# Optimization experiments

Hardware: AMD Instinct MI355X
Metric: run time of the kernel (lower is better)

The kernel has to match this reference:

```python
import jax, jax.numpy as jnp
import numpy as np

F = 39          # total fields = 13 numeric + 26 categorical
NUM_NUM = 13
N_CAT = 26
V = 100000      # vocab per categorical field
E = 16          # embed size
RED = max(1, F // 3)  # SE reduction size = 13
P = F * (F - 1) // 2  # 741 pairs
HID = [1024, 512, 256]
B = 4096

I_IDX, J_IDX = np.triu_indices(F, k=1)  # static pair indices, len P


def setup_inputs() -> dict:
    key = jax.random.key(0)
    ks = jax.random.split(key, 16)
    s = 0.01
    inp = {
        "cat": jax.random.randint(ks[0], (B, N_CAT), 0, V),
        "num": jax.random.normal(ks[1], (B, NUM_NUM), dtype=jnp.float32),
        "embed_tables": jax.random.normal(ks[2], (N_CAT, V, E), dtype=jnp.float32) * s,
        "num_emb": jax.random.normal(ks[3], (NUM_NUM, E), dtype=jnp.float32) * s,
        "W_se1": jax.random.normal(ks[4], (F, RED), dtype=jnp.float32) * 0.1,
        "W_se2": jax.random.normal(ks[5], (RED, F), dtype=jnp.float32) * 0.1,
        "W_bil": jax.random.normal(ks[6], (F, E, E), dtype=jnp.float32) * 0.1,  # per-field Linear(E,E,no bias), [field,in,out]
        "W_d1": jax.random.normal(ks[7], (2 * P * E, HID[0]), dtype=jnp.float32) * 0.01,
        "b_d1": jnp.zeros((HID[0],), dtype=jnp.float32),
        "W_d2": jax.random.normal(ks[8], (HID[0], HID[1]), dtype=jnp.float32) * 0.02,
        "b_d2": jnp.zeros((HID[1],), dtype=jnp.float32),
        "W_d3": jax.random.normal(ks[9], (HID[1], HID[2]), dtype=jnp.float32) * 0.02,
        "b_d3": jnp.zeros((HID[2],), dtype=jnp.float32),
        "W_out": jax.random.normal(ks[10], (HID[2], 1), dtype=jnp.float32) * 0.02,
        "b_out": jnp.zeros((1,), dtype=jnp.float32),
    }
    return inp


def _bilinear_each(x, W_bil):
    # x: [B,F,E]; project each field with its own matrix, then pairwise multiply.
    proj = jnp.einsum("bfe,fed->bfd", x, W_bil)            # [B,F,E]
    return proj[:, I_IDX, :] * x[:, J_IDX, :]               # [B,P,E]


def reference(cat, num, embed_tables, num_emb, W_se1, W_se2, W_bil,
              W_d1, b_d1, W_d2, b_d2, W_d3, b_d3, W_out, b_out):
    # categorical embeddings: per-field gather -> [B, N_CAT, E]
    cat_embed = embed_tables[jnp.arange(N_CAT)[None, :], cat]
    # numerical "embeddings": value * learned vector -> [B, NUM_NUM, E]
    num_embed = num[:, :, None] * num_emb[None, :, :]
    x = jnp.concatenate([num_embed, cat_embed], axis=1)     # [B,F,E]

    # SENET gating
    Z = jnp.mean(x, axis=-1)                                 # [B,F]
    A = jax.nn.relu(jax.nn.relu(Z @ W_se1) @ W_se2)          # [B,F]
    V = x * A[:, :, None]

    se_bi = _bilinear_each(V, W_bil)                         # [B,P,E]
    bi = _bilinear_each(x, W_bil)                            # [B,P,E]
    hid = jnp.concatenate([se_bi, bi], axis=1).reshape(x.shape[0], -1)  # [B, 2*P*E]

    h = jax.nn.relu(hid @ W_d1 + b_d1)
    h = jax.nn.relu(h @ W_d2 + b_d2)
    h = jax.nn.relu(h @ W_d3 + b_d3)
    return h @ W_out + b_out                                 # [B,1]
```

## Files before the change

### kernel.cpp

```cpp
#include <hip/hip_runtime.h>

typedef unsigned short u16;
typedef __attribute__((ext_vector_type(8))) __bf16 bf16x8;
typedef __attribute__((ext_vector_type(4))) float f32x4;
typedef __attribute__((ext_vector_type(4))) unsigned short u16x4;
typedef __attribute__((ext_vector_type(8))) unsigned short u16x8;

#define NF    39
#define NNUM  13
#define NCAT  26
#define VOC   100000
#define NPAIR 741
#define KHID  23712
#define BATCH 4096
#define HD1   1024
#define HD2   512
#define HD3   256

__device__ __forceinline__ u16 f2bf(float f) {
  unsigned u = __builtin_bit_cast(unsigned, f);
  return (u16)((u + 0x7fffu + ((u >> 16) & 1u)) >> 16);
}

__device__ __forceinline__ void gload16(const void* g, void* l) {
  __builtin_amdgcn_global_load_lds((const __attribute__((address_space(1))) void*)g,
                                   (__attribute__((address_space(3))) void*)l, 16, 0, 0);
}

__global__ __launch_bounds__(256) void fuse_front(
    const int* __restrict__ cat, const float* __restrict__ num,
    const float* __restrict__ tables, const float* __restrict__ nemb,
    const float* __restrict__ Wse1, const float* __restrict__ Wse2,
    const float* __restrict__ Wbil, u16* __restrict__ hid)
{
  __shared__ float xs[2][NF][16];
  __shared__ float wb[NF][16][16];
  __shared__ float pr[2][NF][16];
  __shared__ float Zs[2][NF], Ts[2][NNUM], As[2][NF];
  __shared__ unsigned char pis[NPAIR], pjs[NPAIR];

  const int b0 = blockIdx.x * 2;
  const int tid = threadIdx.x;

  for (int i = tid; i < NF * 64; i += 256)
    ((f32x4*)wb)[i] = ((const f32x4*)Wbil)[i];

  for (int t = tid; t < 2 * NNUM * 16; t += 256) {
    int r = t / (NNUM * 16), t2 = t % (NNUM * 16);
    int f = t2 >> 4, e = t2 & 15;
    xs[r][f][e] = num[(b0 + r) * NNUM + f] * nemb[t2];
  }
  for (int t = tid; t < 2 * NCAT * 16; t += 256) {
    int r = t / (NCAT * 16), t2 = t % (NCAT * 16);
    int c = t2 >> 4, e = t2 & 15;
    int cv = cat[(b0 + r) * NCAT + c];
    xs[r][NNUM + c][e] = tables[((size_t)c * VOC + cv) * 16 + e];
  }
  for (int p = tid; p < NPAIR; p += 256) {
    int i = 0, rs = 0;
    while (p >= rs + (NF - 1 - i)) { rs += NF - 1 - i; ++i; }
    pis[p] = (unsigned char)i;
    pjs[p] = (unsigned char)(i + 1 + (p - rs));
  }
  __syncthreads();

  if (tid < 2 * NF) {
    int r = tid / NF, f = tid % NF;
    float s = 0.f;
    #pragma unroll
    for (int e = 0; e < 16; ++e) s += xs[r][f][e];
    Zs[r][f] = s * (1.f / 16.f);
  }
  __syncthreads();
  if (tid < 2 * NNUM) {
    int r = tid / NNUM, o = tid % NNUM;
    float s = 0.f;
    for (int f = 0; f < NF; ++f) s += Zs[r][f] * Wse1[f * NNUM + o];
    Ts[r][o] = fmaxf(s, 0.f);
  }
  __syncthreads();
  if (tid < 2 * NF) {
    int r = tid / NF, f = tid % NF;
    float s = 0.f;
    for (int q = 0; q < NNUM; ++q) s += Ts[r][q] * Wse2[q * NF + f];
    As[r][f] = fmaxf(s, 0.f);
  }
  for (int t = tid; t < 2 * NF * 16; t += 256) {
    int r = t / (NF * 16), t2 = t % (NF * 16);
    int f = t2 >> 4, d = t2 & 15;
    float s = 0.f;
    #pragma unroll
    for (int e = 0; e < 16; ++e) s += xs[r][f][e] * wb[f][e][d];
    pr[r][f][d] = s;
  }
  __syncthreads();

  for (int idx = tid; idx < 2 * NPAIR * 2; idx += 256) {
    const int r = idx / (NPAIR * 2), idx2 = idx % (NPAIR * 2);
    const int p = idx2 >> 1, e0 = (idx2 & 1) * 8;
    const int i = pis[p], j = pjs[p];
    const float aa = As[r][i] * As[r][j];
    u16* hr = hid + (size_t)(b0 + r) * KHID;
    u16x8 vb, vs;
    #pragma unroll
    for (int e = 0; e < 8; ++e) {
      float bv = pr[r][i][e0 + e] * xs[r][j][e0 + e];
      vb[e] = f2bf(bv);
      vs[e] = f2bf(aa * bv);
    }
    *reinterpret_cast<u16x8*>(hr + NPAIR * 16 + p * 16 + e0) = vb;
    *reinterpret_cast<u16x8*>(hr + p * 16 + e0) = vs;
  }
}

__global__ __launch_bounds__(256) void transpose_all(
    const float* __restrict__ Wd1, const float* __restrict__ Wd2,
    const float* __restrict__ Wd3, u16* __restrict__ W1t,
    u16* __restrict__ W2t, u16* __restrict__ W3t)
{
  __shared__ float t[32][33];
  const int bid = blockIdx.x;
  const float* in; u16* out; int K, N, kb, nb;
  if (bid < 741 * 32)        { in = Wd1; out = W1t; K = KHID; N = HD1; kb = bid % 741; nb = bid / 741; }
  else if (bid < 741 * 32 + 512) { int r = bid - 741 * 32; in = Wd2; out = W2t; K = HD1; N = HD2; kb = r % 32; nb = r / 32; }
  else                       { int r = bid - 741 * 32 - 512; in = Wd3; out = W3t; K = HD2; N = HD3; kb = r % 16; nb = r / 16; }

  const int k0 = kb * 32, n0 = nb * 32;
  const int c = threadIdx.x & 31, r = threadIdx.x >> 5;
  #pragma unroll
  for (int it = 0; it < 4; ++it)
    t[r + it * 8][c] = in[(size_t)(k0 + r + it * 8) * N + n0 + c];
  __syncthreads();
  const int n = threadIdx.x >> 3, kq = (threadIdx.x & 7) * 4;
  u16x4 v;
  #pragma unroll
  for (int q = 0; q < 4; ++q) v[q] = f2bf(t[kq + q][n]);
  *reinterpret_cast<u16x4*>(out + (size_t)(n0 + n) * K + k0 + kq) = v;
}

__global__ __launch_bounds__(512, 2) void gemm8p_bf16(
    const u16* __restrict__ A, const u16* __restrict__ Bt,
    float* __restrict__ Cp, int M, int N, int K, int totku, int kpb)
{
  __shared__ __align__(16) u16 lds[65536];

  const int tid = threadIdx.x;
  const int wid = tid >> 6, lane = tid & 63;

  const int d = blockIdx.x;
  const int x = d & 7, jj = d >> 3;
  const int mb = ((x & 3) << 2) | (jj & 3);
  const int nb = (jj >> 2) & 3;
  const int sb = ((x >> 2) << 1) | (jj >> 4);

  const int ks0 = sb * kpb;
  const int kunits = (totku - ks0 < kpb) ? (totku - ks0) : kpb;
  const int ftiles = kunits >> 1;

  const int wm = wid >> 2, wn = wid & 3;
  const int lrow = lane & 15, c0 = lane >> 4;

  const int rr = tid >> 2, cc = tid & 3, csrc = cc ^ ((rr >> 1) & 3);
  const u16* pAg = A  + (size_t)((size_t)mb * 256 + rr) * K + (size_t)ks0 * 32 + csrc * 8;
  const u16* pBg = Bt + (size_t)((size_t)nb * 256 + rr) * K + (size_t)ks0 * 32 + csrc * 8;
  const size_t rsk = (size_t)128 * K;
  const int dstoff = tid * 8;

  int offA[8], offB[4];
  #pragma unroll
  for (int m = 0; m < 8; ++m) {
    int r = wm * 128 + m * 16 + lrow;
    offA[m] = r * 32 + ((c0 ^ ((r >> 1) & 3)) << 3);
  }
  #pragma unroll
  for (int n = 0; n < 4; ++n) {
    int r = wn * 64 + n * 16 + lrow;
    offB[n] = r * 32 + ((c0 ^ ((r >> 1) & 3)) << 3);
  }

#define STAGE_A(g) { int sg = ((g) < kunits) ? (g) : (kunits - 1);          \
    const u16* s_ = pAg + (size_t)sg * 32;                                   \
    u16* dp_ = lds + (((g) & 3) * 8192) + dstoff;                            \
    gload16(s_, dp_); gload16(s_ + rsk, dp_ + 4096); }
#define STAGE_B(g) { int sg = ((g) < kunits) ? (g) : (kunits - 1);          \
    const u16* s_ = pBg + (size_t)sg * 32;                                   \
    u16* dp_ = lds + 32768 + (((g) & 3) * 8192) + dstoff;                    \
    gload16(s_, dp_); gload16(s_ + rsk, dp_ + 4096); }

  f32x4 acc[8][4];
  #pragma unroll
  for (int m = 0; m < 8; ++m)
    #pragma unroll
    for (int n = 0; n < 4; ++n) acc[m][n] = f32x4{0.f, 0.f, 0.f, 0.f};

  STAGE_A(0); STAGE_B(0); STAGE_A(1); STAGE_B(1); STAGE_A(2); STAGE_B(2); STAGE_B(3);
  asm volatile("s_waitcnt vmcnt(6)" ::: "memory");
  __builtin_amdgcn_s_barrier();

  bf16x8 a0, a1, a2, a3, bg0, bg1, bg2, bg3;

  for (int tt = 0; tt < ftiles; ++tt) {
    const int g0 = tt << 1;
    const u16* As0 = lds + ((g0 & 3) * 8192);
    const u16* As1 = lds + (((g0 + 1) & 3) * 8192);
    const u16* Bs0 = lds + 32768 + ((g0 & 3) * 8192);
    const u16* Bs1 = lds + 32768 + (((g0 + 1) & 3) * 8192);

    a0 = *reinterpret_cast<const bf16x8*>(As0 + offA[0]);
    a1 = *reinterpret_cast<const bf16x8*>(As0 + offA[1]);
    a2 = *reinterpret_cast<const bf16x8*>(As0 + offA[2]);
    a3 = *reinterpret_cast<const bf16x8*>(As0 + offA[3]);
    bg0 = *reinterpret_cast<const bf16x8*>(Bs0 + offB[0]);
    bg1 = *reinterpret_cast<const bf16x8*>(Bs0 + offB[1]);
    bg2 = *reinterpret_cast<const bf16x8*>(Bs0 + offB[2]);
    bg3 = *reinterpret_cast<const bf16x8*>(Bs0 + offB[3]);
    STAGE_A(g0 + 3);
    __builtin_amdgcn_sched_barrier(0);
    __builtin_amdgcn_s_barrier();
    asm volatile("s_waitcnt lgkmcnt(0)" ::: "memory");
    __builtin_amdgcn_sched_barrier(0);
    __builtin_amdgcn_s_setprio(1);
    acc[0][0] = __builtin_amdgcn_mfma_f32_16x16x32_bf16(a0, bg0, acc[0][0], 0, 0, 0);
    acc[0][1] = __builtin_amdgcn_mfma_f32_16x16x32_bf16(a0, bg1, acc[0][1], 0, 0, 0);
    acc[0][2] = __builtin_amdgcn_mfma_f32_16x16x32_bf16(a0, bg2, acc[0][2], 0, 0, 0);
    acc[0][3] = __builtin_amdgcn_mfma_f32_16x16x32_bf16(a0, bg3, acc[0][3], 0, 0, 0);
    acc[1][0] = __builtin_amdgcn_mfma_f32_16x16x32_bf16(a1, bg0, acc[1][0], 0, 0, 0);
    acc[1][1] = __builtin_amdgcn_mfma_f32_16x16x32_bf16(a1, bg1, acc[1][1], 0, 0, 0);
    acc[1][2] = __builtin_amdgcn_mfma_f32_16x16x32_bf16(a1, bg2, acc[1][2], 0, 0, 0);
    acc[1][3] = __builtin_amdgcn_mfma_f32_16x16x32_bf16(a1, bg3, acc[1][3], 0, 0, 0);
    acc[2][0] = __builtin_amdgcn_mfma_f32_16x16x32_bf16(a2, bg0, acc[2][0], 0, 0, 0);
    acc[2][1] = __builtin_amdgcn_mfma_f32_16x16x32_bf16(a2, bg1, acc[2][1], 0, 0, 0);
    acc[2][2] = __builtin_amdgcn_mfma_f32_16x16x32_bf16(a2, bg2, acc[2][2], 0, 0, 0);
    acc[2][3] = __builtin_amdgcn_mfma_f32_16x16x32_bf16(a2, bg3, acc[2][3], 0, 0, 0);
    acc[3][0] = __builtin_amdgcn_mfma_f32_16x16x32_bf16(a3, bg0, acc[3][0], 0, 0, 0);
    acc[3][1] = __builtin_amdgcn_mfma_f32_16x16x32_bf16(a3, bg1, acc[3][1], 0, 0, 0);
    acc[3][2] = __builtin_amdgcn_mfma_f32_16x16x32_bf16(a3, bg2, acc[3][2], 0, 0, 0);
    acc[3][3] = __builtin_amdgcn_mfma_f32_16x16x32_bf16(a3, bg3, acc[3][3], 0, 0, 0);
    __builtin_amdgcn_s_setprio(0);
    __builtin_amdgcn_sched_barrier(0);
    __builtin_amdgcn_s_barrier();

    a0 = *reinterpret_cast<const bf16x8*>(As0 + offA[4]);
    a1 = *reinterpret_cast<const bf16x8*>(As0 + offA[5]);
    a2 = *reinterpret_cast<const bf16x8*>(As0 + offA[6]);
    a3 = *reinterpret_cast<const bf16x8*>(As0 + offA[7]);
    STAGE_B(g0 + 4);
    __builtin_amdgcn_sched_barrier(0);
    __builtin_amdgcn_s_barrier();
    asm volatile("s_waitcnt lgkmcnt(0)" ::: "memory");
    __builtin_amdgcn_sched_barrier(0);
    __builtin_amdgcn_s_setprio(1);
    acc[4][0] = __builtin_amdgcn_mfma_f32_16x16x32_bf16(a0, bg0, acc[4][0], 0, 0, 0);
    acc[4][1] = __builtin_amdgcn_mfma_f32_16x16x32_bf16(a0, bg1, acc[4][1], 0, 0, 0);
    acc[4][2] = __builtin_amdgcn_mfma_f32_16x16x32_bf16(a0, bg2, acc[4][2], 0, 0, 0);
    acc[4][3] = __builtin_amdgcn_mfma_f32_16x16x32_bf16(a0, bg3, acc[4][3], 0, 0, 0);
    acc[5][0] = __builtin_amdgcn_mfma_f32_16x16x32_bf16(a1, bg0, acc[5][0], 0, 0, 0);
    acc[5][1] = __builtin_amdgcn_mfma_f32_16x16x32_bf16(a1, bg1, acc[5][1], 0, 0, 0);
    acc[5][2] = __builtin_amdgcn_mfma_f32_16x16x32_bf16(a1, bg2, acc[5][2], 0, 0, 0);
    acc[5][3] = __builtin_amdgcn_mfma_f32_16x16x32_bf16(a1, bg3, acc[5][3], 0, 0, 0);
    acc[6][0] = __builtin_amdgcn_mfma_f32_16x16x32_bf16(a2, bg0, acc[6][0], 0, 0, 0);
    acc[6][1] = __builtin_amdgcn_mfma_f32_16x16x32_bf16(a2, bg1, acc[6][1], 0, 0, 0);
    acc[6][2] = __builtin_amdgcn_mfma_f32_16x16x32_bf16(a2, bg2, acc[6][2], 0, 0, 0);
    acc[6][3] = __builtin_amdgcn_mfma_f32_16x16x32_bf16(a2, bg3, acc[6][3], 0, 0, 0);
    acc[7][0] = __builtin_amdgcn_mfma_f32_16x16x32_bf16(a3, bg0, acc[7][0], 0, 0, 0);
    acc[7][1] = __builtin_amdgcn_mfma_f32_16x16x32_bf16(a3, bg1, acc[7][1], 0, 0, 0);
    acc[7][2] = __builtin_amdgcn_mfma_f32_16x16x32_bf16(a3, bg2, acc[7][2], 0, 0, 0);
    acc[7][3] = __builtin_amdgcn_mfma_f32_16x16x32_bf16(a3, bg3, acc[7][3], 0, 0, 0);
    __builtin_amdgcn_s_setprio(0);
    __builtin_amdgcn_sched_barrier(0);
    __builtin_amdgcn_s_barrier();

    a0 = *reinterpret_cast<const bf16x8*>(As1 + offA[0]);
    a1 = *reinterpret_cast<const bf16x8*>(As1 + offA[1]);
    a2 = *reinterpret_cast<const bf16x8*>(As1 + offA[2]);
    a3 = *reinterpret_cast<const bf16x8*>(As1 + offA[3]);
    bg0 = *reinterpret_cast<const bf16x8*>(Bs1 + offB[0]);
    bg1 = *reinterpret_cast<const bf16x8*>(Bs1 + offB[1]);
    bg2 = *reinterpret_cast<const bf16x8*>(Bs1 + offB[2]);
    bg3 = *reinterpret_cast<const bf16x8*>(Bs1 + offB[3]);
    STAGE_A(g0 + 4);
    __builtin_amdgcn_sched_barrier(0);
    __builtin_amdgcn_s_barrier();
    asm volatile("s_waitcnt lgkmcnt(0)" ::: "memory");
    __builtin_amdgcn_sched_barrier(0);
    __builtin_amdgcn_s_setprio(1);
    acc[0][0] = __builtin_amdgcn_mfma_f32_16x16x32_bf16(a0, bg0, acc[0][0], 0, 0, 0);
    acc[0][1] = __builtin_amdgcn_mfma_f32_16x16x32_bf16(a0, bg1, acc[0][1], 0, 0, 0);
    acc[0][2] = __builtin_amdgcn_mfma_f32_16x16x32_bf16(a0, bg2, acc[0][2], 0, 0, 0);
    acc[0][3] = __builtin_amdgcn_mfma_f32_16x16x32_bf16(a0, bg3, acc[0][3], 0, 0, 0);
    acc[1][0] = __builtin_amdgcn_mfma_f32_16x16x32_bf16(a1, bg0, acc[1][0], 0, 0, 0);
    acc[1][1] = __builtin_amdgcn_mfma_f32_16x16x32_bf16(a1, bg1, acc[1][1], 0, 0, 0);
    acc[1][2] = __builtin_amdgcn_mfma_f32_16x16x32_bf16(a1, bg2, acc[1][2], 0, 0, 0);
    acc[1][3] = __builtin_amdgcn_mfma_f32_16x16x32_bf16(a1, bg3, acc[1][3], 0, 0, 0);
    acc[2][0] = __builtin_amdgcn_mfma_f32_16x16x32_bf16(a2, bg0, acc[2][0], 0, 0, 0);
    acc[2][1] = __builtin_amdgcn_mfma_f32_16x16x32_bf16(a2, bg1, acc[2][1], 0, 0, 0);
    acc[2][2] = __builtin_amdgcn_mfma_f32_16x16x32_bf16(a2, bg2, acc[2][2], 0, 0, 0);
    acc[2][3] = __builtin_amdgcn_mfma_f32_16x16x32_bf16(a2, bg3, acc[2][3], 0, 0, 0);
    acc[3][0] = __builtin_amdgcn_mfma_f32_16x16x32_bf16(a3, bg0, acc[3][0], 0, 0, 0);
    acc[3][1] = __builtin_amdgcn_mfma_f32_16x16x32_bf16(a3, bg1, acc[3][1], 0, 0, 0);
    acc[3][2] = __builtin_amdgcn_mfma_f32_16x16x32_bf16(a3, bg2, acc[3][2], 0, 0, 0);
    acc[3][3] = __builtin_amdgcn_mfma_f32_16x16x32_bf16(a3, bg3, acc[3][3], 0, 0, 0);
    __builtin_amdgcn_s_setprio(0);
    __builtin_amdgcn_sched_barrier(0);
    __builtin_amdgcn_s_barrier();

    a0 = *reinterpret_cast<const bf16x8*>(As1 + offA[4]);
    a1 = *reinterpret_cast<const bf16x8*>(As1 + offA[5]);
    a2 = *reinterpret_cast<const bf16x8*>(As1 + offA[6]);
    a3 = *reinterpret_cast<const bf16x8*>(As1 + offA[7]);
    STAGE_B(g0 + 5);
    __builtin_amdgcn_sched_barrier(0);
    __builtin_amdgcn_s_barrier();
    asm volatile("s_waitcnt lgkmcnt(0)" ::: "memory");
    __builtin_amdgcn_sched_barrier(0);
    __builtin_amdgcn_s_setprio(1);
    acc[4][0] = __builtin_amdgcn_mfma_f32_16x16x32_bf16(a0, bg0, acc[4][0], 0, 0, 0);
    acc[4][1] = __builtin_amdgcn_mfma_f32_16x16x32_bf16(a0, bg1, acc[4][1], 0, 0, 0);
    acc[4][2] = __builtin_amdgcn_mfma_f32_16x16x32_bf16(a0, bg2, acc[4][2], 0, 0, 0);
    acc[4][3] = __builtin_amdgcn_mfma_f32_16x16x32_bf16(a0, bg3, acc[4][3], 0, 0, 0);
    acc[5][0] = __builtin_amdgcn_mfma_f32_16x16x32_bf16(a1, bg0, acc[5][0], 0, 0, 0);
    acc[5][1] = __builtin_amdgcn_mfma_f32_16x16x32_bf16(a1, bg1, acc[5][1], 0, 0, 0);
    acc[5][2] = __builtin_amdgcn_mfma_f32_16x16x32_bf16(a1, bg2, acc[5][2], 0, 0, 0);
    acc[5][3] = __builtin_amdgcn_mfma_f32_16x16x32_bf16(a1, bg3, acc[5][3], 0, 0, 0);
    acc[6][0] = __builtin_amdgcn_mfma_f32_16x16x32_bf16(a2, bg0, acc[6][0], 0, 0, 0);
    acc[6][1] = __builtin_amdgcn_mfma_f32_16x16x32_bf16(a2, bg1, acc[6][1], 0, 0, 0);
    acc[6][2] = __builtin_amdgcn_mfma_f32_16x16x32_bf16(a2, bg2, acc[6][2], 0, 0, 0);
    acc[6][3] = __builtin_amdgcn_mfma_f32_16x16x32_bf16(a2, bg3, acc[6][3], 0, 0, 0);
    acc[7][0] = __builtin_amdgcn_mfma_f32_16x16x32_bf16(a3, bg0, acc[7][0], 0, 0, 0);
    acc[7][1] = __builtin_amdgcn_mfma_f32_16x16x32_bf16(a3, bg1, acc[7][1], 0, 0, 0);
    acc[7][2] = __builtin_amdgcn_mfma_f32_16x16x32_bf16(a3, bg2, acc[7][2], 0, 0, 0);
    acc[7][3] = __builtin_amdgcn_mfma_f32_16x16x32_bf16(a3, bg3, acc[7][3], 0, 0, 0);
    __builtin_amdgcn_s_setprio(0);
    __builtin_amdgcn_sched_barrier(0);
    asm volatile("s_waitcnt vmcnt(6)" ::: "memory");
    __builtin_amdgcn_s_barrier();
  }

  if (kunits & 1) {
    asm volatile("s_waitcnt vmcnt(0)" ::: "memory");
    __builtin_amdgcn_s_barrier();
    const int g = kunits - 1;
    const u16* As = lds + ((g & 3) * 8192);
    const u16* Bs = lds + 32768 + ((g & 3) * 8192);
    bg0 = *reinterpret_cast<const bf16x8*>(Bs + offB[0]);
    bg1 = *reinterpret_cast<const bf16x8*>(Bs + offB[1]);
    bg2 = *reinterpret_cast<const bf16x8*>(Bs + offB[2]);
    bg3 = *reinterpret_cast<const bf16x8*>(Bs + offB[3]);
    #pragma unroll
    for (int m = 0; m < 8; ++m) {
      bf16x8 am = *reinterpret_cast<const bf16x8*>(As + offA[m]);
      acc[m][0] = __builtin_amdgcn_mfma_f32_16x16x32_bf16(am, bg0, acc[m][0], 0, 0, 0);
      acc[m][1] = __builtin_amdgcn_mfma_f32_16x16x32_bf16(am, bg1, acc[m][1], 0, 0, 0);
      acc[m][2] = __builtin_amdgcn_mfma_f32_16x16x32_bf16(am, bg2, acc[m][2], 0, 0, 0);
      acc[m][3] = __builtin_amdgcn_mfma_f32_16x16x32_bf16(am, bg3, acc[m][3], 0, 0, 0);
    }
  }
#undef STAGE_A
#undef STAGE_B

  float* C = Cp + (size_t)sb * M * N;
  #pragma unroll
  for (int m = 0; m < 8; ++m) {
    const int rb = mb * 256 + wm * 128 + m * 16 + (lane >> 4) * 4;
    #pragma unroll
    for (int n = 0; n < 4; ++n) {
      const int col = nb * 256 + wn * 64 + n * 16 + (lane & 15);
      #pragma unroll
      for (int j2 = 0; j2 < 4; ++j2)
        __builtin_nontemporal_store(acc[m][n][j2], &C[(size_t)(rb + j2) * N + col]);
    }
  }
}

__global__ __launch_bounds__(256) void gemm_bf16(
    const u16* __restrict__ A, const u16* __restrict__ Bt,
    float* __restrict__ Cp, int M, int N, int K, int kps)
{
  __shared__ __align__(16) u16 lA[128 * 32];
  __shared__ __align__(16) u16 lB[128 * 32];
  const int tid = threadIdx.x;
  const int mb = blockIdx.x, nb = blockIdx.y, sb = blockIdx.z;
  const int w = tid >> 6, lane = tid & 63;
  const int wr = (w >> 1) * 64, wc = (w & 1) * 64;
  const int lrow = lane & 15, lko = (lane >> 4) * 8;

  f32x4 acc[4][4];
  #pragma unroll
  for (int m = 0; m < 4; ++m)
    #pragma unroll
    for (int n = 0; n < 4; ++n) acc[m][n] = f32x4{0.f, 0.f, 0.f, 0.f};

  const u16* Ab = A + (size_t)mb * 128 * K;
  const u16* Bb = Bt + (size_t)nb * 128 * K;
  const int r0 = tid >> 2, inn = (tid & 3) * 8;
  const int l0 = (tid & ~63) * 8, l1 = ((256 + tid) & ~63) * 8;

  const int ks1 = (sb + 1) * kps;
  for (int ks = sb * kps; ks < ks1; ++ks) {
    const int k0 = ks * 32;
    __syncthreads();
    gload16(Ab + (size_t)r0 * K + k0 + inn,        lA + l0);
    gload16(Ab + (size_t)(r0 + 64) * K + k0 + inn, lA + l1);
    gload16(Bb + (size_t)r0 * K + k0 + inn,        lB + l0);
    gload16(Bb + (size_t)(r0 + 64) * K + k0 + inn, lB + l1);
    __syncthreads();
    bf16x8 af[4], bg[4];
    #pragma unroll
    for (int m = 0; m < 4; ++m)
      af[m] = *reinterpret_cast<const bf16x8*>(&lA[(wr + m * 16 + lrow) * 32 + lko]);
    #pragma unroll
    for (int n = 0; n < 4; ++n)
      bg[n] = *reinterpret_cast<const bf16x8*>(&lB[(wc + n * 16 + lrow) * 32 + lko]);
    #pragma unroll
    for (int m = 0; m < 4; ++m)
      #pragma unroll
      for (int n = 0; n < 4; ++n)
        acc[m][n] = __builtin_amdgcn_mfma_f32_16x16x32_bf16(af[m], bg[n], acc[m][n], 0, 0, 0);
  }

  float* C = Cp + (size_t)sb * M * N;
  #pragma unroll
  for (int m = 0; m < 4; ++m) {
    const int rb = mb * 128 + wr + m * 16 + (lane >> 4) * 4;
    #pragma unroll
    for (int n = 0; n < 4; ++n) {
      const int col = nb * 128 + wc + n * 16 + (lane & 15);
      #pragma unroll
      for (int j = 0; j < 4; ++j)
        __builtin_nontemporal_store(acc[m][n][j], &C[(size_t)(rb + j) * N + col]);
    }
  }
}

__global__ __launch_bounds__(256) void reduce_bias_relu_bf16(
    const float* __restrict__ part, int S, size_t MN,
    const float* __restrict__ bias, int nmask, u16* __restrict__ out)
{
  const size_t n8 = MN >> 3;
  for (size_t i8 = blockIdx.x * 256ull + threadIdx.x; i8 < n8; i8 += (size_t)gridDim.x * 256) {
    const size_t base = i8 * 8;
    f32x4 lo = {0.f, 0.f, 0.f, 0.f}, hi = {0.f, 0.f, 0.f, 0.f};
    for (int k = 0; k < S; ++k) {
      const float* p = part + (size_t)k * MN + base;
      f32x4 a = __builtin_nontemporal_load(reinterpret_cast<const f32x4*>(p));
      f32x4 b = __builtin_nontemporal_load(reinterpret_cast<const f32x4*>(p + 4));
      lo += a; hi += b;
    }
    const int bb = (int)(base & (size_t)nmask);
    const f32x4 b0 = *reinterpret_cast<const f32x4*>(bias + bb);
    const f32x4 b1 = *reinterpret_cast<const f32x4*>(bias + bb + 4);
    u16x8 v;
    #pragma unroll
    for (int e = 0; e < 4; ++e) v[e] = f2bf(fmaxf(lo[e] + b0[e], 0.f));
    #pragma unroll
    for (int e = 0; e < 4; ++e) v[4 + e] = f2bf(fmaxf(hi[e] + b1[e], 0.f));
    *reinterpret_cast<u16x8*>(out + base) = v;
  }
}

__global__ __launch_bounds__(256) void reduce3_final(
    const float* __restrict__ part, const float* __restrict__ bd3,
    const float* __restrict__ Wout, const float* __restrict__ bout,
    float* __restrict__ out)
{
  const int row = blockIdx.x * 4 + (threadIdx.x >> 6);
  const int lane = threadIdx.x & 63;
  const size_t MN = (size_t)BATCH * HD3;
  const size_t base = (size_t)row * HD3;
  float s = 0.f;
  #pragma unroll
  for (int i = 0; i < 4; ++i) {
    const int e = lane + i * 64;
    float v = 0.f;
    #pragma unroll
    for (int k = 0; k < 4; ++k)
      v += __builtin_nontemporal_load(&part[(size_t)k * MN + base + e]);
    v = fmaxf(v + bd3[e], 0.f);
    s += v * Wout[e];
  }
  #pragma unroll
  for (int off = 32; off; off >>= 1) s += __shfl_down(s, off, 64);
  if (lane == 0) out[row] = s + bout[0];
}

extern "C" void kernel_launch(void* const* d_in, const int* in_sizes, int n_in,
                              void* d_out, int out_size, void* d_ws, size_t ws_size,
                              hipStream_t stream)
{
  const int*   cat    = (const int*)  d_in[0];
  const float* num    = (const float*)d_in[1];
  const float* tables = (const float*)d_in[2];
  const float* nemb   = (const float*)d_in[3];
  const float* Wse1   = (const float*)d_in[4];
  const float* Wse2   = (const float*)d_in[5];
  const float* Wbil   = (const float*)d_in[6];
  const float* Wd1    = (const float*)d_in[7];
  const float* bd1    = (const float*)d_in[8];
  const float* Wd2    = (const float*)d_in[9];
  const float* bd2    = (const float*)d_in[10];
  const float* Wd3    = (const float*)d_in[11];
  const float* bd3    = (const float*)d_in[12];
  const float* Wout   = (const float*)d_in[13];
  const float* bout   = (const float*)d_in[14];

  char* ws = (char*)d_ws;
  u16*   hid  = (u16*)  (ws + 0ull);
  u16*   W1t  = (u16*)  (ws + 194248704ull);
  float* part = (float*)(ws + 242810880ull);
  u16*   W2t  = (u16*)  (ws + 309919744ull);
  u16*   W3t  = (u16*)  (ws + 310968320ull);
  u16*   h1b  = (u16*)  (ws + 0ull);
  u16*   h2b  = (u16*)  (ws + 8388608ull);

  transpose_all<<<741 * 32 + 512 + 128, 256, 0, stream>>>(Wd1, Wd2, Wd3, W1t, W2t, W3t);
  fuse_front<<<BATCH / 2, 256, 0, stream>>>(cat, num, tables, nemb, Wse1, Wse2, Wbil, hid);

  gemm8p_bf16<<<256, 512, 0, stream>>>(hid, W1t, part, BATCH, HD1, KHID, 741, 186);
  reduce_bias_relu_bf16<<<2048, 256, 0, stream>>>(part, 4, (size_t)BATCH * HD1, bd1, HD1 - 1, h1b);

  gemm_bf16<<<dim3(BATCH / 128, HD2 / 128, 2), 256, 0, stream>>>(h1b, W2t, part, BATCH, HD2, HD1, 16);
  reduce_bias_relu_bf16<<<1024, 256, 0, stream>>>(part, 2, (size_t)BATCH * HD2, bd2, HD2 - 1, h2b);

  gemm_bf16<<<dim3(BATCH / 128, HD3 / 128, 4), 256, 0, stream>>>(h2b, W3t, part, BATCH, HD3, HD2, 4);
  reduce3_final<<<BATCH / 4, 256, 0, stream>>>(part, bd3, Wout, bout, (float*)d_out);
}
```

Before: 332.4 us.

## Software-pipeline LDS fragment loads one MFMA phase ahead in GEMM main loop

```diff
diff --git a/kernel.cpp b/kernel.cpp
--- a/kernel.cpp
+++ b/kernel.cpp
@@ -197,143 +197,155 @@
   asm volatile("s_waitcnt vmcnt(6)" ::: "memory");
   __builtin_amdgcn_s_barrier();
 
-  bf16x8 a0, a1, a2, a3, bg0, bg1, bg2, bg3;
+  bf16x8 ac0, ac1, ac2, ac3, an0, an1, an2, an3;
+  bf16x8 bgc0, bgc1, bgc2, bgc3, bgn0, bgn1, bgn2, bgn3;
+
+  {
+    const u16* As0_ = lds;
+    const u16* Bs0_ = lds + 32768;
+    ac0 = *reinterpret_cast<const bf16x8*>(As0_ + offA[0]);
+    ac1 = *reinterpret_cast<const bf16x8*>(As0_ + offA[1]);
+    ac2 = *reinterpret_cast<const bf16x8*>(As0_ + offA[2]);
+    ac3 = *reinterpret_cast<const bf16x8*>(As0_ + offA[3]);
+    bgc0 = *reinterpret_cast<const bf16x8*>(Bs0_ + offB[0]);
+    bgc1 = *reinterpret_cast<const bf16x8*>(Bs0_ + offB[1]);
+    bgc2 = *reinterpret_cast<const bf16x8*>(Bs0_ + offB[2]);
+    bgc3 = *reinterpret_cast<const bf16x8*>(Bs0_ + offB[3]);
+  }
 
   for (int tt = 0; tt < ftiles; ++tt) {
     const int g0 = tt << 1;
     const u16* As0 = lds + ((g0 & 3) * 8192);
     const u16* As1 = lds + (((g0 + 1) & 3) * 8192);
-    const u16* Bs0 = lds + 32768 + ((g0 & 3) * 8192);
     const u16* Bs1 = lds + 32768 + (((g0 + 1) & 3) * 8192);
-
-    a0 = *reinterpret_cast<const bf16x8*>(As0 + offA[0]);
-    a1 = *reinterpret_cast<const bf16x8*>(As0 + offA[1]);
-    a2 = *reinterpret_cast<const bf16x8*>(As0 + offA[2]);
-    a3 = *reinterpret_cast<const bf16x8*>(As0 + offA[3]);
-    bg0 = *reinterpret_cast<const bf16x8*>(Bs0 + offB[0]);
-    bg1 = *reinterpret_cast<const bf16x8*>(Bs0 + offB[1]);
-    bg2 = *reinterpret_cast<const bf16x8*>(Bs0 + offB[2]);
-    bg3 = *reinterpret_cast<const bf16x8*>(Bs0 + offB[3]);
+    const u16* As2 = lds + (((g0 + 2) & 3) * 8192);
+    const u16* Bs2 = lds + 32768 + (((g0 + 2) & 3) * 8192);
+
+    __builtin_amdgcn_s_barrier();
     STAGE_A(g0 + 3);
-    __builtin_amdgcn_sched_barrier(0);
+    an0 = *reinterpret_cast<const bf16x8*>(As0 + offA[4]);
+    an1 = *reinterpret_cast<const bf16x8*>(As0 + offA[5]);
+    an2 = *reinterpret_cast<const bf16x8*>(As0 + offA[6]);
+    an3 = *reinterpret_cast<const bf16x8*>(As0 + offA[7]);
+    __builtin_amdgcn_sched_barrier(0);
+    asm volatile("s_waitcnt lgkmcnt(4)" ::: "memory");
+    __builtin_amdgcn_sched_barrier(0);
+    __builtin_amdgcn_s_setprio(1);
+    acc[0][0] = __builtin_amdgcn_mfma_f32_16x16x32_bf16(ac0, bgc0, acc[0][0], 0, 0, 0);
+    acc[0][1] = __builtin_amdgcn_mfma_f32_16x16x32_bf16(ac0, bgc1, acc[0][1], 0, 0, 0);
+    acc[0][2] = __builtin_amdgcn_mfma_f32_16x16x32_bf16(ac0, bgc2, acc[0][2], 0, 0, 0);
+    acc[0][3] = __builtin_amdgcn_mfma_f32_16x16x32_bf16(ac0, bgc3, acc[0][3], 0, 0, 0);
+    acc[1][0] = __builtin_amdgcn_mfma_f32_16x16x32_bf16(ac1, bgc0, acc[1][0], 0, 0, 0);
+    acc[1][1] = __builtin_amdgcn_mfma_f32_16x16x32_bf16(ac1, bgc1, acc[1][1], 0, 0, 0);
+    acc[1][2] = __builtin_amdgcn_mfma_f32_16x16x32_bf16(ac1, bgc2, acc[1][2], 0, 0, 0);
+    acc[1][3] = __builtin_amdgcn_mfma_f32_16x16x32_bf16(ac1, bgc3, acc[1][3], 0, 0, 0);
+    acc[2][0] = __builtin_amdgcn_mfma_f32_16x16x32_bf16(ac2, bgc0, acc[2][0], 0, 0, 0);
+    acc[2][1] = __builtin_amdgcn_mfma_f32_16x16x32_bf16(ac2, bgc1, acc[2][1], 0, 0, 0);
+    acc[2][2] = __builtin_amdgcn_mfma_f32_16x16x32_bf16(ac2, bgc2, acc[2][2], 0, 0, 0);
+    acc[2][3] = __builtin_amdgcn_mfma_f32_16x16x32_bf16(ac2, bgc3, acc[2][3], 0, 0, 0);
+    acc[3][0] = __builtin_amdgcn_mfma_f32_16x16x32_bf16(ac3, bgc0, acc[3][0], 0, 0, 0);
+    acc[3][1] = __builtin_amdgcn_mfma_f32_16x16x32_bf16(ac3, bgc1, acc[3][1], 0, 0, 0);
+    acc[3][2] = __builtin_amdgcn_mfma_f32_16x16x32_bf16(ac3, bgc2, acc[3][2], 0, 0, 0);
+    acc[3][3] = __builtin_amdgcn_mfma_f32_16x16x32_bf16(ac3, bgc3, acc[3][3], 0, 0, 0);
+    __builtin_amdgcn_s_setprio(0);
+    __builtin_amdgcn_sched_barrier(0);
+
     __builtin_amdgcn_s_barrier();
-    asm volatile("s_waitcnt lgkmcnt(0)" ::: "memory");
+    STAGE_B(g0 + 4);
+    ac0 = *reinterpret_cast<const bf16x8*>(As1 + offA[0]);
+    ac1 = *reinterpret_cast<const bf16x8*>(As1 + offA[1]);
+    ac2 = *reinterpret_cast<const bf16x8*>(As1 + offA[2]);
+    ac3 = *reinterpret_cast<const bf16x8*>(As1 + offA[3]);
+    bgn0 = *reinterpret_cast<const bf16x8*>(Bs1 + offB[0]);
+    bgn1 = *reinterpret_cast<const bf16x8*>(Bs1 + offB[1]);
+    bgn2 = *reinterpret_cast<const bf16x8*>(Bs1 + offB[2]);
+    bgn3 = *reinterpret_cast<const bf16x8*>(Bs1 + offB[3]);
+    __builtin_amdgcn_sched_barrier(0);
+    asm volatile("s_waitcnt lgkmcnt(8)" ::: "memory");
     __builtin_amdgcn_sched_barrier(0);
     __builtin_amdgcn_s_setprio(1);
-    acc[0][0] = __builtin_amdgcn_mfma_f32_16x16x32_bf16(a0, bg0, acc[0][0], 0, 0, 0);
-    acc[0][1] = __builtin_amdgcn_mfma_f32_16x16x32_bf16(a0, bg1, acc[0][1], 0, 0, 0);
-    acc[0][2] = __builtin_amdgcn_mfma_f32_16x16x32_bf16(a0, bg2, acc[0][2], 0, 0, 0);
-    acc[0][3] = __builtin_amdgcn_mfma_f32_16x16x32_bf16(a0, bg3, acc[0][3], 0, 0, 0);
-    acc[1][0] = __builtin_amdgcn_mfma_f32_16x16x32_bf16(a1, bg0, acc[1][0], 0, 0, 0);
-    acc[1][1] = __builtin_amdgcn_mfma_f32_16x16x32_bf16(a1, bg1, acc[1][1], 0, 0, 0);
-    acc[1][2] = __builtin_amdgcn_mfma_f32_16x16x32_bf16(a1, bg2, acc[1][2], 0, 0, 0);
-    acc[1][3] = __builtin_amdgcn_mfma_f32_16x16x32_bf16(a1, bg3, acc[1][3], 0, 0, 0);
-    acc[2][0] = __builtin_amdgcn_mfma_f32_16x16x32_bf16(a2, bg0, acc[2][0], 0, 0, 0);
-    acc[2][1] = __builtin_amdgcn_mfma_f32_16x16x32_bf16(a2, bg1, acc[2][1], 0, 0, 0);
-    acc[2][2] = __builtin_amdgcn_mfma_f32_16x16x32_bf16(a2, bg2, acc[2][2], 0, 0, 0);
-    acc[2][3] = __builtin_amdgcn_mfma_f32_16x16x32_bf16(a2, bg3, acc[2][3], 0, 0, 0);
-    acc[3][0] = __builtin_amdgcn_mfma_f32_16x16x32_bf16(a3, bg0, acc[3][0], 0, 0, 0);
-    acc[3][1] = __builtin_amdgcn_mfma_f32_16x16x32_bf16(a3, bg1, acc[3][1], 0, 0, 0);
-    acc[3][2] = __builtin_amdgcn_mfma_f32_16x16x32_bf16(a3, bg2, acc[3][2], 0, 0, 0);
-    acc[3][3] = __builtin_amdgcn_mfma_f32_16x16x32_bf16(a3, bg3, acc[3][3], 0, 0, 0);
+    acc[4][0] = __builtin_amdgcn_mfma_f32_16x16x32_bf16(an0, bgc0, acc[4][0], 0, 0, 0);
+    acc[4][1] = __builtin_amdgcn_mfma_f32_16x16x32_bf16(an0, bgc1, acc[4][1], 0, 0, 0);
+    acc[4][2] = __builtin_amdgcn_mfma_f32_16x16x32_bf16(an0, bgc2, acc[4][2], 0, 0, 0);
+    acc[4][3] = __builtin_amdgcn_mfma_f32_16x16x32_bf16(an0, bgc3, acc[4][3], 0, 0, 0);
+    acc[5][0] = __builtin_amdgcn_mfma_f32_16x16x32_bf16(an1, bgc0, acc[5][0], 0, 0, 0);
+    acc[5][1] = __builtin_amdgcn_mfma_f32_16x16x32_bf16(an1, bgc1, acc[5][1], 0, 0, 0);
+    acc[5][2] = __builtin_amdgcn_mfma_f32_16x16x32_bf16(an1, bgc2, acc[5][2], 0, 0, 0);
+    acc[5][3] = __builtin_amdgcn_mfma_f32_16x16x32_bf16(an1, bgc3, acc[5][3], 0, 0, 0);
+    acc[6][0] = __builtin_amdgcn_mfma_f32_16x16x32_bf16(an2, bgc0, acc[6][0], 0, 0, 0);
+    acc[6][1] = __builtin_amdgcn_mfma_f32_16x16x32_bf16(an2, bgc1, acc[6][1], 0, 0, 0);
+    acc[6][2] = __builtin_amdgcn_mfma_f32_16x16x32_bf16(an2, bgc2, acc[6][2], 0, 0, 0);
+    acc[6][3] = __builtin_amdgcn_mfma_f32_16x16x32_bf16(an2, bgc3, acc[6][3], 0, 0, 0);
+    acc[7][0] = __builtin_amdgcn_mfma_f32_16x16x32_bf16(an3, bgc0, acc[7][0], 0, 0, 0);
+    acc[7][1] = __builtin_amdgcn_mfma_f32_16x16x32_bf16(an3, bgc1, acc[7][1], 0, 0, 0);
+    acc[7][2] = __builtin_amdgcn_mfma_f32_16x16x32_bf16(an3, bgc2, acc[7][2], 0, 0, 0);
+    acc[7][3] = __builtin_amdgcn_mfma_f32_16x16x32_bf16(an3, bgc3, acc[7][3], 0, 0, 0);
     __builtin_amdgcn_s_setprio(0);
     __builtin_amdgcn_sched_barrier(0);
+
     __builtin_amdgcn_s_barrier();
-
-    a0 = *reinterpret_cast<const bf16x8*>(As0 + offA[4]);
-    a1 = *reinterpret_cast<const bf16x8*>(As0 + offA[5]);
-    a2 = *reinterpret_cast<const bf16x8*>(As0 + offA[6]);
-    a3 = *reinterpret_cast<const bf16x8*>(As0 + offA[7]);
-    STAGE_B(g0 + 4);
-    __builtin_amdgcn_sched_barrier(0);
+    STAGE_A(g0 + 4);
+    an0 = *reinterpret_cast<const bf16x8*>(As1 + offA[4]);
+    an1 = *reinterpret_cast<const bf16x8*>(As1 + offA[5]);
+    an2 = *reinterpret_cast<const bf16x8*>(As1 + offA[6]);
+    an3 = *reinterpret_cast<const bf16x8*>(As1 + offA[7]);
+    __builtin_amdgcn_sched_barrier(0);
+    asm volatile("s_waitcnt lgkmcnt(4)" ::: "memory");
+    __builtin_amdgcn_sched_barrier(0);
+    __builtin_amdgcn_s_setprio(1);
+    acc[0][0] = __builtin_amdgcn_mfma_f32_16x16x32_bf16(ac0, bgn0, acc[0][0], 0, 0, 0);
+    acc[0][1] = __builtin_amdgcn_mfma_f32_16x16x32_bf16(ac0, bgn1, acc[0][1], 0, 0, 0);
+    acc[0][2] = __builtin_amdgcn_mfma_f32_16x16x32_bf16(ac0, bgn2, acc[0][2], 0, 0, 0);
+    acc[0][3] = __builtin_amdgcn_mfma_f32_16x16x32_bf16(ac0, bgn3, acc[0][3], 0, 0, 0);
+    acc[1][0] = __builtin_amdgcn_mfma_f32_16x16x32_bf16(ac1, bgn0, acc[1][0], 0, 0, 0);
+    acc[1][1] = __builtin_amdgcn_mfma_f32_16x16x32_bf16(ac1, bgn1, acc[1][1], 0, 0, 0);
+    acc[1][2] = __builtin_amdgcn_mfma_f32_16x16x32_bf16(ac1, bgn2, acc[1][2], 0, 0, 0);
+    acc[1][3] = __builtin_amdgcn_mfma_f32_16x16x32_bf16(ac1, bgn3, acc[1][3], 0, 0, 0);
+    acc[2][0] = __builtin_amdgcn_mfma_f32_16x16x32_bf16(ac2, bgn0, acc[2][0], 0, 0, 0);
+    acc[2][1] = __builtin_amdgcn_mfma_f32_16x16x32_bf16(ac2, bgn1, acc[2][1], 0, 0, 0);
+    acc[2][2] = __builtin_amdgcn_mfma_f32_16x16x32_bf16(ac2, bgn2, acc[2][2], 0, 0, 0);
+    acc[2][3] = __builtin_amdgcn_mfma_f32_16x16x32_bf16(ac2, bgn3, acc[2][3], 0, 0, 0);
+    acc[3][0] = __builtin_amdgcn_mfma_f32_16x16x32_bf16(ac3, bgn0, acc[3][0], 0, 0, 0);
+    acc[3][1] = __builtin_amdgcn_mfma_f32_16x16x32_bf16(ac3, bgn1, acc[3][1], 0, 0, 0);
+    acc[3][2] = __builtin_amdgcn_mfma_f32_16x16x32_bf16(ac3, bgn2, acc[3][2], 0, 0, 0);
+    acc[3][3] = __builtin_amdgcn_mfma_f32_16x16x32_bf16(ac3, bgn3, acc[3][3], 0, 0, 0);
+    __builtin_amdgcn_s_setprio(0);
+    __builtin_amdgcn_sched_barrier(0);
+    asm volatile("s_waitcnt vmcnt(6)" ::: "memory");
+
     __builtin_amdgcn_s_barrier();
-    asm volatile("s_waitcnt lgkmcnt(0)" ::: "memory");
+    STAGE_B(g0 + 5);
+    ac0 = *reinterpret_cast<const bf16x8*>(As2 + offA[0]);
+    ac1 = *reinterpret_cast<const bf16x8*>(As2 + offA[1]);
+    ac2 = *reinterpret_cast<const bf16x8*>(As2 + offA[2]);
+    ac3 = *reinterpret_cast<const bf16x8*>(As2 + offA[3]);
+    bgc0 = *reinterpret_cast<const bf16x8*>(Bs2 + offB[0]);
+    bgc1 = *reinterpret_cast<const bf16x8*>(Bs2 + offB[1]);
+    bgc2 = *reinterpret_cast<const bf16x8*>(Bs2 + offB[2]);
+    bgc3 = *reinterpret_cast<const bf16x8*>(Bs2 + offB[3]);
+    __builtin_amdgcn_sched_barrier(0);
+    asm volatile("s_waitcnt lgkmcnt(8)" ::: "memory");
     __builtin_amdgcn_sched_barrier(0);
     __builtin_amdgcn_s_setprio(1);
-    acc[4][0] = __builtin_amdgcn_mfma_f32_16x16x32_bf16(a0, bg0, acc[4][0], 0, 0, 0);
-    acc[4][1] = __builtin_amdgcn_mfma_f32_16x16x32_bf16(a0, bg1, acc[4][1], 0, 0, 0);
-    acc[4][2] = __builtin_amdgcn_mfma_f32_16x16x32_bf16(a0, bg2, acc[4][2], 0, 0, 0);
-    acc[4][3] = __builtin_amdgcn_mfma_f32_16x16x32_bf16(a0, bg3, acc[4][3], 0, 0, 0);
-    acc[5][0] = __builtin_amdgcn_mfma_f32_16x16x32_bf16(a1, bg0, acc[5][0], 0, 0, 0);
-    acc[5][1] = __builtin_amdgcn_mfma_f32_16x16x32_bf16(a1, bg1, acc[5][1], 0, 0, 0);
-    acc[5][2] = __builtin_amdgcn_mfma_f32_16x16x32_bf16(a1, bg2, acc[5][2], 0, 0, 0);
-    acc[5][3] = __builtin_amdgcn_mfma_f32_16x16x32_bf16(a1, bg3, acc[5][3], 0, 0, 0);
-    acc[6][0] = __builtin_amdgcn_mfma_f32_16x16x32_bf16(a2, bg0, acc[6][0], 0, 0, 0);
-    acc[6][1] = __builtin_amdgcn_mfma_f32_16x16x32_bf16(a2, bg1, acc[6][1], 0, 0, 0);
-    acc[6][2] = __builtin_amdgcn_mfma_f32_16x16x32_bf16(a2, bg2, acc[6][2], 0, 0, 0);
-    acc[6][3] = __builtin_amdgcn_mfma_f32_16x16x32_bf16(a2, bg3, acc[6][3], 0, 0, 0);
-    acc[7][0] = __builtin_amdgcn_mfma_f32_16x16x32_bf16(a3, bg0, acc[7][0], 0, 0, 0);
-    acc[7][1] = __builtin_amdgcn_mfma_f32_16x16x32_bf16(a3, bg1, acc[7][1], 0, 0, 0);
-    acc[7][2] = __builtin_amdgcn_mfma_f32_16x16x32_bf16(a3, bg2, acc[7][2], 0, 0, 0);
-    acc[7][3] = __builtin_amdgcn_mfma_f32_16x16x32_bf16(a3, bg3, acc[7][3], 0, 0, 0);
+    acc[4][0] = __builtin_amdgcn_mfma_f32_16x16x32_bf16(an0, bgn0, acc[4][0], 0, 0, 0);
+    acc[4][1] = __builtin_amdgcn_mfma_f32_16x16x32_bf16(an0, bgn1, acc[4][1], 0, 0, 0);
+    acc[4][2] = __builtin_amdgcn_mfma_f32_16x16x32_bf16(an0, bgn2, acc[4][2], 0, 0, 0);
+    acc[4][3] = __builtin_amdgcn_mfma_f32_16x16x32_bf16(an0, bgn3, acc[4][3], 0, 0, 0);
+    acc[5][0] = __builtin_amdgcn_mfma_f32_16x16x32_bf16(an1, bgn0, acc[5][0], 0, 0, 0);
+    acc[5][1] = __builtin_amdgcn_mfma_f32_16x16x32_bf16(an1, bgn1, acc[5][1], 0, 0, 0);
+    acc[5][2] = __builtin_amdgcn_mfma_f32_16x16x32_bf16(an1, bgn2, acc[5][2], 0, 0, 0);
+    acc[5][3] = __builtin_amdgcn_mfma_f32_16x16x32_bf16(an1, bgn3, acc[5][3], 0, 0, 0);
+    acc[6][0] = __builtin_amdgcn_mfma_f32_16x16x32_bf16(an2, bgn0, acc[6][0], 0, 0, 0);
+    acc[6][1] = __builtin_amdgcn_mfma_f32_16x16x32_bf16(an2, bgn1, acc[6][1], 0, 0, 0);
+    acc[6][2] = __builtin_amdgcn_mfma_f32_16x16x32_bf16(an2, bgn2, acc[6][2], 0, 0, 0);
+    acc[6][3] = __builtin_amdgcn_mfma_f32_16x16x32_bf16(an2, bgn3, acc[6][3], 0, 0, 0);
+    acc[7][0] = __builtin_amdgcn_mfma_f32_16x16x32_bf16(an3, bgn0, acc[7][0], 0, 0, 0);
+    acc[7][1] = __builtin_amdgcn_mfma_f32_16x16x32_bf16(an3, bgn1, acc[7][1], 0, 0, 0);
+    acc[7][2] = __builtin_amdgcn_mfma_f32_16x16x32_bf16(an3, bgn2, acc[7][2], 0, 0, 0);
+    acc[7][3] = __builtin_amdgcn_mfma_f32_16x16x32_bf16(an3, bgn3, acc[7][3], 0, 0, 0);
     __builtin_amdgcn_s_setprio(0);
     __builtin_amdgcn_sched_barrier(0);
-    __builtin_amdgcn_s_barrier();
-
-    a0 = *reinterpret_cast<const bf16x8*>(As1 + offA[0]);
-    a1 = *reinterpret_cast<const bf16x8*>(As1 + offA[1]);
-    a2 = *reinterpret_cast<const bf16x8*>(As1 + offA[2]);
-    a3 = *reinterpret_cast<const bf16x8*>(As1 + offA[3]);
-    bg0 = *reinterpret_cast<const bf16x8*>(Bs1 + offB[0]);
-    bg1 = *reinterpret_cast<const bf16x8*>(Bs1 + offB[1]);
-    bg2 = *reinterpret_cast<const bf16x8*>(Bs1 + offB[2]);
-    bg3 = *reinterpret_cast<const bf16x8*>(Bs1 + offB[3]);
-    STAGE_A(g0 + 4);
-    __builtin_amdgcn_sched_barrier(0);
-    __builtin_amdgcn_s_barrier();
-    asm volatile("s_waitcnt lgkmcnt(0)" ::: "memory");
-    __builtin_amdgcn_sched_barrier(0);
-    __builtin_amdgcn_s_setprio(1);
-    acc[0][0] = __builtin_amdgcn_mfma_f32_16x16x32_bf16(a0, bg0, acc[0][0], 0, 0, 0);
-    acc[0][1] = __builtin_amdgcn_mfma_f32_16x16x32_bf16(a0, bg1, acc[0][1], 0, 0, 0);
-    acc[0][2] = __builtin_amdgcn_mfma_f32_16x16x32_bf16(a0, bg2, acc[0][2], 0, 0, 0);
-    acc[0][3] = __builtin_amdgcn_mfma_f32_16x16x32_bf16(a0, bg3, acc[0][3], 0, 0, 0);
-    acc[1][0] = __builtin_amdgcn_mfma_f32_16x16x32_bf16(a1, bg0, acc[1][0], 0, 0, 0);
-    acc[1][1] = __builtin_amdgcn_mfma_f32_16x16x32_bf16(a1, bg1, acc[1][1], 0, 0, 0);
-    acc[1][2] = __builtin_amdgcn_mfma_f32_16x16x32_bf16(a1, bg2, acc[1][2], 0, 0, 0);
-    acc[1][3] = __builtin_amdgcn_mfma_f32_16x16x32_bf16(a1, bg3, acc[1][3], 0, 0, 0);
-    acc[2][0] = __builtin_amdgcn_mfma_f32_16x16x32_bf16(a2, bg0, acc[2][0], 0, 0, 0);
-    acc[2][1] = __builtin_amdgcn_mfma_f32_16x16x32_bf16(a2, bg1, acc[2][1], 0, 0, 0);
-    acc[2][2] = __builtin_amdgcn_mfma_f32_16x16x32_bf16(a2, bg2, acc[2][2], 0, 0, 0);
-    acc[2][3] = __builtin_amdgcn_mfma_f32_16x16x32_bf16(a2, bg3, acc[2][3], 0, 0, 0);
-    acc[3][0] = __builtin_amdgcn_mfma_f32_16x16x32_bf16(a3, bg0, acc[3][0], 0, 0, 0);
-    acc[3][1] = __builtin_amdgcn_mfma_f32_16x16x32_bf16(a3, bg1, acc[3][1], 0, 0, 0);
-    acc[3][2] = __builtin_amdgcn_mfma_f32_16x16x32_bf16(a3, bg2, acc[3][2], 0, 0, 0);
-    acc[3][3] = __builtin_amdgcn_mfma_f32_16x16x32_bf16(a3, bg3, acc[3][3], 0, 0, 0);
-    __builtin_amdgcn_s_setprio(0);
-    __builtin_amdgcn_sched_barrier(0);
-    __builtin_amdgcn_s_barrier();
-
-    a0 = *reinterpret_cast<const bf16x8*>(As1 + offA[4]);
-    a1 = *reinterpret_cast<const bf16x8*>(As1 + offA[5]);
-    a2 = *reinterpret_cast<const bf16x8*>(As1 + offA[6]);
-    a3 = *reinterpret_cast<const bf16x8*>(As1 + offA[7]);
-    STAGE_B(g0 + 5);
-    __builtin_amdgcn_sched_barrier(0);
-    __builtin_amdgcn_s_barrier();
-    asm volatile("s_waitcnt lgkmcnt(0)" ::: "memory");
-    __builtin_amdgcn_sched_barrier(0);
-    __builtin_amdgcn_s_setprio(1);
-    acc[4][0] = __builtin_amdgcn_mfma_f32_16x16x32_bf16(a0, bg0, acc[4][0], 0, 0, 0);
-    acc[4][1] = __builtin_amdgcn_mfma_f32_16x16x32_bf16(a0, bg1, acc[4][1], 0, 0, 0);
-    acc[4][2] = __builtin_amdgcn_mfma_f32_16x16x32_bf16(a0, bg2, acc[4][2], 0, 0, 0);
-    acc[4][3] = __builtin_amdgcn_mfma_f32_16x16x32_bf16(a0, bg3, acc[4][3], 0, 0, 0);
-    acc[5][0] = __builtin_amdgcn_mfma_f32_16x16x32_bf16(a1, bg0, acc[5][0], 0, 0, 0);
-    acc[5][1] = __builtin_amdgcn_mfma_f32_16x16x32_bf16(a1, bg1, acc[5][1], 0, 0, 0);
-    acc[5][2] = __builtin_amdgcn_mfma_f32_16x16x32_bf16(a1, bg2, acc[5][2], 0, 0, 0);
-    acc[5][3] = __builtin_amdgcn_mfma_f32_16x16x32_bf16(a1, bg3, acc[5][3], 0, 0, 0);
-    acc[6][0] = __builtin_amdgcn_mfma_f32_16x16x32_bf16(a2, bg0, acc[6][0], 0, 0, 0);
-    acc[6][1] = __builtin_amdgcn_mfma_f32_16x16x32_bf16(a2, bg1, acc[6][1], 0, 0, 0);
-    acc[6][2] = __builtin_amdgcn_mfma_f32_16x16x32_bf16(a2, bg2, acc[6][2], 0, 0, 0);
-    acc[6][3] = __builtin_amdgcn_mfma_f32_16x16x32_bf16(a2, bg3, acc[6][3], 0, 0, 0);
-    acc[7][0] = __builtin_amdgcn_mfma_f32_16x16x32_bf16(a3, bg0, acc[7][0], 0, 0, 0);
-    acc[7][1] = __builtin_amdgcn_mfma_f32_16x16x32_bf16(a3, bg1, acc[7][1], 0, 0, 0);
-    acc[7][2] = __builtin_amdgcn_mfma_f32_16x16x32_bf16(a3, bg2, acc[7][2], 0, 0, 0);
-    acc[7][3] = __builtin_amdgcn_mfma_f32_16x16x32_bf16(a3, bg3, acc[7][3], 0, 0, 0);
-    __builtin_amdgcn_s_setprio(0);
-    __builtin_amdgcn_sched_barrier(0);
     asm volatile("s_waitcnt vmcnt(6)" ::: "memory");
-    __builtin_amdgcn_s_barrier();
   }
 
   if (kunits & 1) {
@@ -342,17 +354,17 @@
     const int g = kunits - 1;
     const u16* As = lds + ((g & 3) * 8192);
     const u16* Bs = lds + 32768 + ((g & 3) * 8192);
-    bg0 = *reinterpret_cast<const bf16x8*>(Bs + offB[0]);
-    bg1 = *reinterpret_cast<const bf16x8*>(Bs + offB[1]);
-    bg2 = *reinterpret_cast<const bf16x8*>(Bs + offB[2]);
-    bg3 = *reinterpret_cast<const bf16x8*>(Bs + offB[3]);
+    bf16x8 tb0 = *reinterpret_cast<const bf16x8*>(Bs + offB[0]);
+    bf16x8 tb1 = *reinterpret_cast<const bf16x8*>(Bs + offB[1]);
+    bf16x8 tb2 = *reinterpret_cast<const bf16x8*>(Bs + offB[2]);
+    bf16x8 tb3 = *reinterpret_cast<const bf16x8*>(Bs + offB[3]);
     #pragma unroll
     for (int m = 0; m < 8; ++m) {
       bf16x8 am = *reinterpret_cast<const bf16x8*>(As + offA[m]);
-      acc[m][0] = __builtin_amdgcn_mfma_f32_16x16x32_bf16(am, bg0, acc[m][0], 0, 0, 0);
-      acc[m][1] = __builtin_amdgcn_mfma_f32_16x16x32_bf16(am, bg1, acc[m][1], 0, 0, 0);
-      acc[m][2] = __builtin_amdgcn_mfma_f32_16x16x32_bf16(am, bg2, acc[m][2], 0, 0, 0);
-      acc[m][3] = __builtin_amdgcn_mfma_f32_16x16x32_bf16(am, bg3, acc[m][3], 0, 0, 0);
+      acc[m][0] = __builtin_amdgcn_mfma_f32_16x16x32_bf16(am, tb0, acc[m][0], 0, 0, 0);
+      acc[m][1] = __builtin_amdgcn_mfma_f32_16x16x32_bf16(am, tb1, acc[m][1], 0, 0, 0);
+      acc[m][2] = __builtin_amdgcn_mfma_f32_16x16x32_bf16(am, tb2, acc[m][2], 0, 0, 0);
+      acc[m][3] = __builtin_amdgcn_mfma_f32_16x16x32_bf16(am, tb3, acc[m][3], 0, 0, 0);
     }
   }
 #undef STAGE_A
```

Result: slower. 342.1 us (+2.9%).
